# Optimization experiments

Hardware: AMD Instinct MI355X
Metric: run time of the kernel (lower is better)

## Reference

```python
import jax, jax.numpy as jnp
import numpy as np

KER = 8  # patch size used by unfold/fold
EPS = 1e-5


def _gelu(x):
    return jax.nn.gelu(x, approximate=False)  # torch nn.GELU default (exact erf)


def _conv(x, w, b):
    # x: [B,C,H,W], w: [O,I,kh,kw]
    y = jax.lax.conv_general_dilated(x, w, (1, 1), 'SAME',
                                     dimension_numbers=('NCHW', 'OIHW', 'NCHW'))
    return y + b[None, :, None, None]


def _unfold_t(x):
    # F.unfold(k=8, s=8).transpose(1,2): [B,C,H,W] -> [B, L, C*k*k]
    B, C, H, W = x.shape
    Hp, Wp = H // KER, W // KER
    x = x.reshape(B, C, Hp, KER, Wp, KER)
    x = x.transpose(0, 2, 4, 1, 3, 5)  # [B,Hp,Wp,C,k,k]
    return x.reshape(B, Hp * Wp, C * KER * KER)


def _fold(y, H, W):
    # inverse of unfold (non-overlapping): [B,L,C*k*k] -> [B,C,H,W]
    B, L, D = y.shape
    Hp, Wp = H // KER, W // KER
    C = D // (KER * KER)
    y = y.reshape(B, Hp, Wp, C, KER, KER).transpose(0, 3, 1, 4, 2, 5)
    return y.reshape(B, C, H, W)


def _bn1d(x, gamma, beta):
    # BatchNorm1d (training-mode batch stats) on [B, C, L]: stats over (B, L)
    m = x.mean(axis=(0, 2), keepdims=True)
    v = x.var(axis=(0, 2), keepdims=True)  # biased variance, matches torch fwd
    return (x - m) * jax.lax.rsqrt(v + EPS) * gamma[None, :, None] + beta[None, :, None]


def setup_inputs() -> dict:
    key = jax.random.key(0)
    ks = jax.random.split(key, 12)
    B, C, H, W = 4, 64, 256, 256
    dq = KER * KER * C  # 4096

    def n(k, shape, scale=0.02):
        return jax.random.normal(k, shape, jnp.float32) * scale

    return {
        'feat': jax.random.normal(ks[0], (B, C, H, W), jnp.float32),
        'w_enc': n(ks[1], (C, C, 3, 3)), 'b_enc': jnp.zeros((C,), jnp.float32),
        'w_kc': n(ks[2], (C, C, 3, 3)), 'b_kc': jnp.zeros((C,), jnp.float32),
        'w_vc': n(ks[3], (C, C, 3, 3)), 'b_vc': jnp.zeros((C,), jnp.float32),
        'wq': n(ks[4], (1024, dq)), 'bq': jnp.zeros((1024,), jnp.float32),
        'wk': n(ks[5], (1024, dq)), 'bk': jnp.zeros((1024,), jnp.float32),
        'gq': jnp.ones((1024,), jnp.float32), 'betaq': jnp.zeros((1024,), jnp.float32),
        'gk': jnp.ones((1024,), jnp.float32), 'betak': jnp.zeros((1024,), jnp.float32),
        'w_f1': n(ks[6], (4 * C, C, 1, 1)), 'b_f1': jnp.zeros((4 * C,), jnp.float32),
        'w_f2': n(ks[7], (C, 4 * C, 1, 1)), 'b_f2': jnp.zeros((C,), jnp.float32),
    }


def reference(feat, w_enc, b_enc, w_kc, b_kc, w_vc, b_vc, wq, bq, wk, bk,
              gq, betaq, gk, betak, w_f1, b_f1, w_f2, b_f2):
    H, W = feat.shape[-2:]
    refer = _gelu(_conv(feat, w_enc, b_enc))
    feat_k = _gelu(_conv(feat, w_kc, b_kc))
    feat_v = _gelu(_conv(feat, w_vc, b_vc))

    q_un = _unfold_t(refer)   # [B,L,4096]
    k_un = _unfold_t(feat_k)
    v_un = _unfold_t(feat_v)

    # Linear -> BN1d over 1024 channels (transpose dance as in the torch code)
    qp = _bn1d((q_un @ wq.T + bq).transpose(0, 2, 1), gq, betaq).transpose(0, 2, 1)  # [B,L,1024]
    kp = _bn1d((k_un @ wk.T + bk).transpose(0, 2, 1), gk, betak).transpose(0, 2, 1)  # [B,L,1024]

    scale = jnp.sqrt(jnp.asarray(qp.shape[2], qp.dtype))
    scores = jnp.einsum('bld,bmd->blm', qp, kp) / scale  # [B,L,L]
    attn = jax.nn.softmax(scores, axis=2)
    out = jnp.einsum('blm,bmd->bld', attn, v_un)  # [B,L,4096]

    out = _fold(out, H, W)  # [B,C,H,W]
    ff = _gelu(_conv(out, w_f1, b_f1))
    ff = _gelu(_conv(ff, w_f2, b_f2))
    return ff + feat
```

## Files before the change

### kernel.cpp

```cpp
#include <hip/hip_runtime.h>
#include <hip/hip_bf16.h>

typedef unsigned short u16;
typedef __attribute__((ext_vector_type(8))) short short8v;
typedef __attribute__((ext_vector_type(8))) unsigned short u16x8;
typedef __attribute__((ext_vector_type(4))) float f32x4;

#define HWPIX 65536
#define AS1(p) ((const __attribute__((address_space(1))) void*)(p))
#define AS3(p) ((__attribute__((address_space(3))) void*)(p))

__device__ __forceinline__ float bfbits2f(u16 u) {
  return __uint_as_float(((unsigned)u) << 16);
}
__device__ __forceinline__ float4 ld4bf(const u16* p) {
  ushort4 u = *(const ushort4*)(const void*)p;
  return make_float4(bfbits2f(u.x), bfbits2f(u.y), bfbits2f(u.z), bfbits2f(u.w));
}
__device__ __forceinline__ u16 f2bf(float f) {
  union { __hip_bfloat16 h; u16 u; } c;
  c.h = __float2bfloat16(f);
  return c.u;
}
__device__ __forceinline__ float gelu_f(float x) {
  float z = 0.79788456f * x * (1.0f + 0.044715f * x * x);
  float e = __expf(2.0f * z);
  float th = 1.0f - 2.0f * __builtin_amdgcn_rcpf(e + 1.0f);
  return 0.5f * x * (1.0f + th);
}
__device__ __forceinline__ u16x8 bn8(u16x8 v, const float* __restrict__ sc,
                                     const float* __restrict__ sh, int kk) {
  float4 s0 = *(const float4*)&sc[kk], s1 = *(const float4*)&sc[kk + 4];
  float4 t0 = *(const float4*)&sh[kk], t1 = *(const float4*)&sh[kk + 4];
  u16x8 r;
  r[0] = f2bf(bfbits2f(v[0]) * s0.x + t0.x); r[1] = f2bf(bfbits2f(v[1]) * s0.y + t0.y);
  r[2] = f2bf(bfbits2f(v[2]) * s0.z + t0.z); r[3] = f2bf(bfbits2f(v[3]) * s0.w + t0.w);
  r[4] = f2bf(bfbits2f(v[4]) * s1.x + t1.x); r[5] = f2bf(bfbits2f(v[5]) * s1.y + t1.y);
  r[6] = f2bf(bfbits2f(v[6]) * s1.z + t1.z); r[7] = f2bf(bfbits2f(v[7]) * s1.w + t1.w);
  return r;
}

__launch_bounds__(256)
__global__ void prep_k(const float* __restrict__ feat, u16* __restrict__ featb,
                       const float* __restrict__ w0, const float* __restrict__ w1,
                       const float* __restrict__ w2, const float* __restrict__ b0,
                       const float* __restrict__ b1, const float* __restrict__ b2,
                       const float* __restrict__ wf1, const float* __restrict__ wf2,
                       u16* __restrict__ wT, float* __restrict__ bias192,
                       u16* __restrict__ wf1b, u16* __restrict__ wf2b) {
  __shared__ float tile[64][65];
  const int t = threadIdx.x;
  const int bxg = blockIdx.x;
  if (bxg < 4096) {
    const int xs = (bxg & 3) << 6, yy = (bxg >> 2) & 255, b = bxg >> 10;
#pragma unroll
    for (int it = 0; it < 4; ++it) {
      const int idx = t + it * 256;
      const int c = idx >> 4, seg = (idx & 15) << 2;
      float4 v = *(const float4*)&feat[(((size_t)(b * 64 + c)) << 16) + yy * 256 + xs + seg];
      tile[c][seg] = v.x; tile[c][seg + 1] = v.y; tile[c][seg + 2] = v.z; tile[c][seg + 3] = v.w;
    }
    __syncthreads();
#pragma unroll
    for (int it = 0; it < 4; ++it) {
      const int idx = t + it * 256;
      const int cs = (idx & 15) << 2, px = idx >> 4;
      ushort4 r;
      r.x = f2bf(tile[cs + 0][px]); r.y = f2bf(tile[cs + 1][px]);
      r.z = f2bf(tile[cs + 2][px]); r.w = f2bf(tile[cs + 3][px]);
      *(ushort4*)&featb[(((size_t)((b * 256 + yy) * 256 + xs + px)) << 6) + cs] = r;
    }
    return;
  }
  const int bx = bxg - 4096;
  if (bx >= 497) {
    const int e = (bx - 497) * 256 + t;
    wf2b[e] = f2bf(wf2[e]);
    return;
  }
  if (bx >= 433) {
    const int e = (bx - 433) * 256 + t;
    wf1b[e] = f2bf(wf1[e]);
    return;
  }
  if (bx == 432) {
    if (t < 192) {
      const float* bp = (t < 64) ? b0 : (t < 128) ? b1 : b2;
      bias192[t] = bp[t & 63];
    }
    return;
  }
  const int e = bx * 256 + t;
  const int pos = e / 12288, rem = e % 12288;
  const int n = rem >> 6, ic = rem & 63;
  const int conv = n >> 6, oc = n & 63;
  const float* wp = (conv == 0) ? w0 : (conv == 1) ? w1 : w2;
  wT[e] = f2bf(wp[(oc * 64 + ic) * 9 + pos]);
}

__launch_bounds__(256)
__global__ void wcvt2_k(const float* __restrict__ s0, u16* __restrict__ d0,
                        const float* __restrict__ s1, u16* __restrict__ d1) {
  const float* src = blockIdx.y ? s1 : s0;
  u16* dst = blockIdx.y ? d1 : d0;
  const int i = (blockIdx.x * 256 + threadIdx.x) << 2;
  float4 v = *(const float4*)&src[i];
  ushort4 r;
  r.x = f2bf(v.x); r.y = f2bf(v.y); r.z = f2bf(v.z); r.w = f2bf(v.w);
  *(ushort4*)&dst[i] = r;
}

__launch_bounds__(256)
__global__ void convmfma_k(const u16* __restrict__ featb, const u16* __restrict__ wT,
                           const float* __restrict__ bias192, u16* __restrict__ qun,
                           u16* __restrict__ kun, u16* __restrict__ vT) {
  __shared__ u16 As[128 * 64];
  __shared__ u16 Bs[192 * 64];
  const int tid = threadIdx.x;
  const int lin = blockIdx.x;
  const int virt = (lin & 7) * 256 + (lin >> 3);
  const int b = virt >> 9, yy = (virt >> 1) & 255, x0 = (virt & 1) << 7;
  const int lane = tid & 63, w = tid >> 6;
  const int wm = w >> 1, wn = w & 1;

  u16x8 rA[4], rB[6];
  auto issue = [&](int pos) {
    const int dy = pos / 3, dx = pos % 3;
    const int yp = yy + dy - 1;
    const bool yok = (unsigned)yp < 256u;
#pragma unroll
    for (int i = 0; i < 4; ++i) {
      const int slot = tid + (i << 8);
      const int row = slot >> 3, cg = slot & 7;
      const int xp = x0 + row + dx - 1;
      u16x8 v{};
      if (yok && (unsigned)xp < 256u)
        v = *(const u16x8*)&featb[(((size_t)((b * 256 + yp) * 256 + xp)) << 6) + (cg << 3)];
      rA[i] = v;
    }
    const u16* wb = wT + (size_t)pos * 12288;
#pragma unroll
    for (int i = 0; i < 6; ++i) {
      const int slot = tid + (i << 8);
      const int row = slot >> 3, cg = slot & 7;
      rB[i] = *(const u16x8*)&wb[(row << 6) + (cg << 3)];
    }
  };
  auto commit = [&]() {
#pragma unroll
    for (int i = 0; i < 4; ++i) {
      const int slot = tid + (i << 8);
      const int row = slot >> 3, cg = slot & 7;
      *(u16x8*)&As[(row << 6) + ((cg ^ (row & 7)) << 3)] = rA[i];
    }
#pragma unroll
    for (int i = 0; i < 6; ++i) {
      const int slot = tid + (i << 8);
      const int row = slot >> 3, cg = slot & 7;
      *(u16x8*)&Bs[(row << 6) + ((cg ^ (row & 7)) << 3)] = rB[i];
    }
  };

  f32x4 acc[4][6] = {};
  const int kc = (lane >> 4) << 3;
  const int afr = wm * 64 + (lane & 15);
  const int bfr0 = wn * 96 + (lane & 15);

  issue(0);
  commit();
  __syncthreads();

  for (int pos = 0; pos < 9; ++pos) {
    if (pos + 1 < 9) issue(pos + 1);
#pragma unroll
    for (int ks = 0; ks < 2; ++ks) {
      const int ce = (ks << 5) + kc;
      short8v a[4], bf[6];
#pragma unroll
      for (int f = 0; f < 4; ++f) {
        const int row = afr + f * 16;
        a[f] = *(const short8v*)&As[(row << 6) + (ce ^ ((row & 7) << 3))];
      }
#pragma unroll
      for (int f = 0; f < 6; ++f) {
        const int row = bfr0 + f * 16;
        bf[f] = *(const short8v*)&Bs[(row << 6) + (ce ^ ((row & 7) << 3))];
      }
#pragma unroll
      for (int i = 0; i < 4; ++i)
#pragma unroll
        for (int j = 0; j < 6; ++j)
          acc[i][j] = __builtin_amdgcn_mfma_f32_16x16x32_bf16(a[i], bf[j], acc[i][j], 0, 0, 0);
    }
    __syncthreads();
    if (pos + 1 < 9) {
      commit();
      __syncthreads();
    }
  }

  const int py = yy >> 3, ky = yy & 7;
  const int rp0 = wm * 64 + ((lane >> 4) << 2);
#pragma unroll
  for (int j = 0; j < 6; ++j) {
    const int colb = wn * 96 + j * 16;
    const int conv = colb >> 6;
    const int oc = (colb & 63) + (lane & 15);
    const float bj = bias192[colb + (lane & 15)];
#pragma unroll
    for (int i = 0; i < 4; ++i) {
      const int rp = rp0 + i * 16;
      const int xg = x0 + rp;
      const int px = xg >> 3, kx0 = xg & 7;
      float v0 = gelu_f(acc[i][j][0] + bj);
      float v1 = gelu_f(acc[i][j][1] + bj);
      float v2 = gelu_f(acc[i][j][2] + bj);
      float v3 = gelu_f(acc[i][j][3] + bj);
      const int d0 = (oc << 6) + (ky << 3) + kx0;
      if (conv < 2) {
        u16* dst = conv ? kun : qun;
        const size_t addr = (((size_t)((b << 10) + py * 32 + px)) << 12) + d0;
        ushort4 r4;
        r4.x = f2bf(v0); r4.y = f2bf(v1); r4.z = f2bf(v2); r4.w = f2bf(v3);
        *(ushort4*)&dst[addr] = r4;
      } else {
        const int m = py * 32 + px;
        const size_t base = (((size_t)(b * 4096 + d0)) << 10) + m;
        vT[base] = f2bf(v0);
        vT[base + 1024] = f2bf(v1);
        vT[base + 2048] = f2bf(v2);
        vT[base + 3072] = f2bf(v3);
      }
    }
  }
}

__launch_bounds__(256)
__global__ void bnpart_k(const u16* __restrict__ q, const u16* __restrict__ k,
                         float2* __restrict__ part) {
  const u16* x = blockIdx.y ? k : q;
  const int b = blockIdx.x, t = threadIdx.x;
  const int c = t << 2;
  float s0 = 0.f, s1 = 0.f, s2 = 0.f, s3 = 0.f;
  float q0 = 0.f, q1 = 0.f, q2 = 0.f, q3 = 0.f;
  const u16* base = x + ((size_t)b << 15) + c;
#pragma unroll 4
  for (int r = 0; r < 32; ++r) {
    float4 v = ld4bf(base + (r << 10));
    s0 += v.x; q0 += v.x * v.x;
    s1 += v.y; q1 += v.y * v.y;
    s2 += v.z; q2 += v.z * v.z;
    s3 += v.w; q3 += v.w * v.w;
  }
  float2* dst = part + (((size_t)(blockIdx.y * 128 + b)) << 10) + c;
  dst[0] = make_float2(s0, q0);
  dst[1] = make_float2(s1, q1);
  dst[2] = make_float2(s2, q2);
  dst[3] = make_float2(s3, q3);
}
__launch_bounds__(256)
__global__ void bnfin_k(const float2* __restrict__ part, const float* __restrict__ gq,
                        const float* __restrict__ betaq, const float* __restrict__ gk,
                        const float* __restrict__ betak, float* __restrict__ scq,
                        float* __restrict__ shq, float* __restrict__ sck,
                        float* __restrict__ shk) {
  const int n = blockIdx.x * 256 + threadIdx.x;
  const int y = blockIdx.y;
  const float2* p = part + (((size_t)(y * 128)) << 10) + n;
  float S = 0.f, S2 = 0.f;
  for (int i = 0; i < 128; ++i) {
    float2 v = p[(size_t)i << 10];
    S += v.x; S2 += v.y;
  }
  const float mean = S * (1.0f / 4096.0f);
  const float var = S2 * (1.0f / 4096.0f) - mean * mean;
  const float rstd = rsqrtf(var + 1e-5f);
  const float g = (y ? gk : gq)[n];
  const float be = (y ? betak : betaq)[n];
  const float sc = g * rstd;
  (y ? sck : scq)[n] = sc;
  (y ? shk : shq)[n] = be - mean * sc;
}

__launch_bounds__(256)
__global__ void softmax_k(u16* __restrict__ s) {
  u16* p = s + (size_t)blockIdx.x * 1024;
  const int tid = threadIdx.x;
  float4 v = ld4bf(p + (tid << 2));
  float mx = fmaxf(fmaxf(v.x, v.y), fmaxf(v.z, v.w));
#pragma unroll
  for (int off = 32; off > 0; off >>= 1) mx = fmaxf(mx, __shfl_xor(mx, off));
  __shared__ float red[8];
  if ((tid & 63) == 0) red[tid >> 6] = mx;
  __syncthreads();
  mx = fmaxf(fmaxf(red[0], red[1]), fmaxf(red[2], red[3]));
  float e0 = __expf(v.x - mx), e1 = __expf(v.y - mx), e2 = __expf(v.z - mx), e3 = __expf(v.w - mx);
  float sm = e0 + e1 + e2 + e3;
#pragma unroll
  for (int off = 32; off > 0; off >>= 1) sm += __shfl_xor(sm, off);
  if ((tid & 63) == 0) red[4 + (tid >> 6)] = sm;
  __syncthreads();
  sm = red[4] + red[5] + red[6] + red[7];
  float inv = 1.0f / sm;
  ushort4 r;
  r.x = f2bf(e0 * inv); r.y = f2bf(e1 * inv); r.z = f2bf(e2 * inv); r.w = f2bf(e3 * inv);
  *(ushort4*)&p[tid << 2] = r;
}

template <int MODE>
__launch_bounds__(512)
__global__ void mgemmL_k(const u16* __restrict__ Ap0, const u16* __restrict__ Bp0,
                         const float* __restrict__ bias0, u16* __restrict__ Cp0, int K,
                         const u16* __restrict__ Ap2, const u16* __restrict__ Bp2,
                         const float* __restrict__ bias2, u16* __restrict__ Cp2) {
  constexpr int SD = (MODE == 0) ? 4096 : 1024;
  __shared__ u16 As[2][128 * 32];
  __shared__ u16 Bs[2][128 * 32];
  const int tid = threadIdx.x;

  int bx, by, z;
  if constexpr (MODE == 2) {
    int lin = blockIdx.x + 32 * blockIdx.y + 256 * blockIdx.z;
    int sw = (lin & 7) * 128 + (lin >> 3);
    bx = sw & 31; by = (sw >> 5) & 7; z = sw >> 8;
  } else {
    bx = blockIdx.x; by = blockIdx.y; z = blockIdx.z;
  }
  const u16* Ap = Ap0;
  const u16* Bp = Bp0;
  const float* bias = bias0;
  u16* Cp = Cp0;
  if constexpr (MODE == 0) {
    if (z) { Ap = Ap2; Bp = Bp2; bias = bias2; Cp = Cp2; }
  }
  const int m0 = by * 128, n0 = bx * 128;
  const int lane = tid & 63, w = tid >> 6;
  const int wm = w >> 2, wn = w & 3;

  const int srow = tid >> 2;
  const int scol = (((tid & 3) ^ ((srow >> 1) & 3)) << 3);
  const size_t zoffA = (MODE == 0) ? 0 : ((size_t)z << 10);
  const size_t zoffB = (MODE == 0) ? 0 : ((size_t)z << 12);
  const u16* gA = Ap + (zoffA + m0 + srow) * (size_t)SD + scol;
  const u16* gB = Bp + (zoffB + n0 + srow) * (size_t)SD + scol;
  const int lwb = w * 512;

  const int NT = K >> 5;
  __builtin_amdgcn_global_load_lds(AS1(gA), AS3(&As[0][lwb]), 16, 0, 0);
  __builtin_amdgcn_global_load_lds(AS1(gB), AS3(&Bs[0][lwb]), 16, 0, 0);

  f32x4 acc[4][2] = {};
  const int fr = lane & 15;
  const int kg = (lane >> 4) << 3;
  const int colsw = kg ^ (((fr >> 1) & 3) << 3);
  int cur = 0;
  for (int t = 0; t < NT; ++t) {
    __syncthreads();
    if (t + 1 < NT) {
      const int kn = (t + 1) << 5;
      __builtin_amdgcn_global_load_lds(AS1(gA + kn), AS3(&As[cur ^ 1][lwb]), 16, 0, 0);
      __builtin_amdgcn_global_load_lds(AS1(gB + kn), AS3(&Bs[cur ^ 1][lwb]), 16, 0, 0);
    }
    const u16* Asb = As[cur];
    const u16* Bsb = Bs[cur];
    short8v a[4], bfr[2];
#pragma unroll
    for (int f = 0; f < 4; ++f)
      a[f] = *(const short8v*)&Asb[(wm * 64 + fr + f * 16) * 32 + colsw];
#pragma unroll
    for (int f = 0; f < 2; ++f)
      bfr[f] = *(const short8v*)&Bsb[(wn * 32 + fr + f * 16) * 32 + colsw];
#pragma unroll
    for (int i = 0; i < 4; ++i)
#pragma unroll
      for (int j = 0; j < 2; ++j)
        acc[i][j] = __builtin_amdgcn_mfma_f32_16x16x32_bf16(a[i], bfr[j], acc[i][j], 0, 0, 0);
    cur ^= 1;
  }

  const int rowbase = m0 + wm * 64 + ((lane >> 4) << 2);
  const int colbase = n0 + wn * 32 + (lane & 15);
  if constexpr (MODE == 2) {
    const size_t coff = (size_t)(8 + 8 * z) * 524288;
    u16* C = Cp + coff;
#pragma unroll
    for (int j = 0; j < 2; ++j) {
      const int d = colbase + j * 16;
      const int c = d >> 6, ky = (d >> 3) & 7, kx = d & 7;
#pragma unroll
      for (int i = 0; i < 4; ++i)
#pragma unroll
        for (int r = 0; r < 4; ++r) {
          const int l = rowbase + i * 16 + r;
          const int p = (((l >> 5) << 3) + ky) * 256 + ((l & 31) << 3) + kx;
          C[((size_t)p << 6) + c] = f2bf(acc[i][j][r]);
        }
    }
  } else {
#pragma unroll
    for (int j = 0; j < 2; ++j) {
      const int col = colbase + j * 16;
      const float bj = bias[col];
#pragma unroll
      for (int i = 0; i < 4; ++i)
#pragma unroll
        for (int r = 0; r < 4; ++r)
          Cp[(size_t)(rowbase + i * 16 + r) * 1024 + col] = f2bf(acc[i][j][r] + bj);
    }
  }
}

__launch_bounds__(512)
__global__ void mgemm1_k(const u16* __restrict__ Ap, const u16* __restrict__ Bp,
                         const float* __restrict__ sA, const float* __restrict__ hA,
                         const float* __restrict__ sB, const float* __restrict__ hB,
                         u16* __restrict__ Cp, int K) {
  constexpr int SD = 1024;
  __shared__ u16 As[2][128 * 72];
  __shared__ u16 Bs[2][128 * 72];
  const int tid = threadIdx.x;
  const int bx = blockIdx.x, by = blockIdx.y, z = blockIdx.z;
  const int m0 = by * 128, n0 = bx * 128;
  const int lane = tid & 63, w = tid >> 6;
  const int wm = w >> 2, wn = w & 3;

  const int srow = tid >> 3;
  const int scol = (tid & 7) << 3;
  const size_t zoff = (size_t)z << 10;
  const u16* A0 = Ap + (zoff + m0 + srow) * (size_t)SD + scol;
  const u16* A1 = A0 + (size_t)64 * SD;
  const u16* B0 = Bp + (zoff + n0 + srow) * (size_t)SD + scol;
  const u16* B1 = B0 + (size_t)64 * SD;
  const int l0 = srow * 72 + scol;
  const int l1 = (srow + 64) * 72 + scol;

  const int NT = K >> 6;
  u16x8 pA0 = bn8(*(const u16x8*)A0, sA, hA, scol);
  u16x8 pA1 = bn8(*(const u16x8*)A1, sA, hA, scol);
  u16x8 pB0 = bn8(*(const u16x8*)B0, sB, hB, scol);
  u16x8 pB1 = bn8(*(const u16x8*)B1, sB, hB, scol);
  *(u16x8*)&As[0][l0] = pA0; *(u16x8*)&As[0][l1] = pA1;
  *(u16x8*)&Bs[0][l0] = pB0; *(u16x8*)&Bs[0][l1] = pB1;
  __syncthreads();

  f32x4 acc[4][2] = {};
  int cur = 0;
  for (int t = 0; t < NT; ++t) {
    const int kn = (t + 1) << 6;
    if (t + 1 < NT) {
      pA0 = *(const u16x8*)(A0 + kn);
      pA1 = *(const u16x8*)(A1 + kn);
      pB0 = *(const u16x8*)(B0 + kn);
      pB1 = *(const u16x8*)(B1 + kn);
    }
    const u16* Asb = As[cur];
    const u16* Bsb = Bs[cur];
#pragma unroll
    for (int ks = 0; ks < 2; ++ks) {
      const int kc = ks * 32 + ((lane >> 4) << 3);
      short8v a[4], bfr[2];
#pragma unroll
      for (int f = 0; f < 4; ++f)
        a[f] = *(const short8v*)&Asb[(wm * 64 + (lane & 15) + f * 16) * 72 + kc];
#pragma unroll
      for (int f = 0; f < 2; ++f)
        bfr[f] = *(const short8v*)&Bsb[(wn * 32 + (lane & 15) + f * 16) * 72 + kc];
#pragma unroll
      for (int i = 0; i < 4; ++i)
#pragma unroll
        for (int j = 0; j < 2; ++j)
          acc[i][j] = __builtin_amdgcn_mfma_f32_16x16x32_bf16(a[i], bfr[j], acc[i][j], 0, 0, 0);
    }
    if (t + 1 < NT) {
      pA0 = bn8(pA0, sA, hA, kn + scol); pA1 = bn8(pA1, sA, hA, kn + scol);
      pB0 = bn8(pB0, sB, hB, kn + scol); pB1 = bn8(pB1, sB, hB, kn + scol);
      *(u16x8*)&As[cur ^ 1][l0] = pA0; *(u16x8*)&As[cur ^ 1][l1] = pA1;
      *(u16x8*)&Bs[cur ^ 1][l0] = pB0; *(u16x8*)&Bs[cur ^ 1][l1] = pB1;
    }
    __syncthreads();
    cur ^= 1;
  }

  const int rowbase = m0 + wm * 64 + ((lane >> 4) << 2);
  const int colbase = n0 + wn * 32 + (lane & 15);
#pragma unroll
  for (int j = 0; j < 2; ++j) {
    const int col = colbase + j * 16;
#pragma unroll
    for (int i = 0; i < 4; ++i)
#pragma unroll
      for (int r = 0; r < 4; ++r) {
        const size_t row = ((size_t)z << 10) + rowbase + i * 16 + r;
        Cp[row * 1024 + col] = f2bf(acc[i][j][r] * 0.03125f);
      }
  }
}

__launch_bounds__(512)
__global__ void ffn_k(const u16* __restrict__ fold, const u16* __restrict__ w1b,
                      const u16* __restrict__ w2b, const float* __restrict__ b1,
                      const float* __restrict__ b2, const float* __restrict__ feat,
                      float* __restrict__ out) {
  extern __shared__ u16 sh[];
  u16* Ash = sh;
  u16* W1s = sh + 9216;
  u16* mids = sh;
  const int t = threadIdx.x;
  const int px0 = blockIdx.x << 7;
  const int z = blockIdx.y;
  const u16* fz = fold + ((size_t)z << 22);

  {
    const int row = t >> 2, cs = (t & 3) << 4;
    const u16* src = fz + (((size_t)(px0 + row)) << 6) + cs;
    *(u16x8*)&Ash[row * 72 + cs] = *(const u16x8*)src;
    *(u16x8*)&Ash[row * 72 + cs + 8] = *(const u16x8*)(src + 8);
  }
  {
    const int row = t >> 1, cs = (t & 1) << 5;
    const u16* src = w1b + (((size_t)row) << 6) + cs;
    *(u16x8*)&W1s[row * 72 + cs] = *(const u16x8*)src;
    *(u16x8*)&W1s[row * 72 + cs + 8] = *(const u16x8*)(src + 8);
    *(u16x8*)&W1s[row * 72 + cs + 16] = *(const u16x8*)(src + 16);
    *(u16x8*)&W1s[row * 72 + cs + 24] = *(const u16x8*)(src + 24);
  }
  __syncthreads();

  const int lane = t & 63, w = t >> 6;
  const int kc = (lane >> 4) << 3;
  const int mrow = w * 16 + (lane & 15);
  f32x4 acc1[16] = {};
  short8v a0 = *(const short8v*)&Ash[mrow * 72 + kc];
  short8v a1 = *(const short8v*)&Ash[mrow * 72 + 32 + kc];
#pragma unroll
  for (int n = 0; n < 16; ++n) {
    const int br = n * 16 + (lane & 15);
    short8v b0 = *(const short8v*)&W1s[br * 72 + kc];
    short8v bv = *(const short8v*)&W1s[br * 72 + 32 + kc];
    acc1[n] = __builtin_amdgcn_mfma_f32_16x16x32_bf16(a0, b0, acc1[n], 0, 0, 0);
    acc1[n] = __builtin_amdgcn_mfma_f32_16x16x32_bf16(a1, bv, acc1[n], 0, 0, 0);
  }
  __syncthreads();

  const int mrow0 = w * 16 + ((lane >> 4) << 2);
#pragma unroll
  for (int n = 0; n < 16; ++n) {
    const int col = n * 16 + (lane & 15);
    const float bj = b1[col];
#pragma unroll
    for (int r = 0; r < 4; ++r)
      mids[(mrow0 + r) * 264 + col] = f2bf(gelu_f(acc1[n][r] + bj));
  }
  __syncthreads();

  f32x4 acc2[4] = {};
#pragma unroll
  for (int ks = 0; ks < 8; ++ks) {
    short8v a2 = *(const short8v*)&mids[(w * 16 + (lane & 15)) * 264 + ks * 32 + kc];
#pragma unroll
    for (int n = 0; n < 4; ++n) {
      short8v bv = *(const short8v*)(const void*)&w2b[(size_t)(n * 16 + (lane & 15)) * 256 + ks * 32 + kc];
      acc2[n] = __builtin_amdgcn_mfma_f32_16x16x32_bf16(a2, bv, acc2[n], 0, 0, 0);
    }
  }
#pragma unroll
  for (int n = 0; n < 4; ++n) {
    const int oc = n * 16 + (lane & 15);
    const float bn = b2[oc];
    const int px = px0 + mrow0;
    const size_t base = (((size_t)(z * 64 + oc)) << 16) + px;
    float4 f = *(const float4*)&feat[base];
    float4 rv;
    rv.x = gelu_f(acc2[n][0] + bn) + f.x;
    rv.y = gelu_f(acc2[n][1] + bn) + f.y;
    rv.z = gelu_f(acc2[n][2] + bn) + f.z;
    rv.w = gelu_f(acc2[n][3] + bn) + f.w;
    *(float4*)&out[base] = rv;
  }
}

extern "C" void kernel_launch(void* const* d_in, const int* in_sizes, int n_in,
                              void* d_out, int out_size, void* d_ws, size_t ws_size,
                              hipStream_t stream) {
  const float* feat  = (const float*)d_in[0];
  const float* w_enc = (const float*)d_in[1];
  const float* b_enc = (const float*)d_in[2];
  const float* w_kc  = (const float*)d_in[3];
  const float* b_kc  = (const float*)d_in[4];
  const float* w_vc  = (const float*)d_in[5];
  const float* b_vc  = (const float*)d_in[6];
  const float* wq    = (const float*)d_in[7];
  const float* bq    = (const float*)d_in[8];
  const float* wk    = (const float*)d_in[9];
  const float* bk    = (const float*)d_in[10];
  const float* gq    = (const float*)d_in[11];
  const float* betaq = (const float*)d_in[12];
  const float* gk    = (const float*)d_in[13];
  const float* betak = (const float*)d_in[14];
  const float* w_f1  = (const float*)d_in[15];
  const float* b_f1  = (const float*)d_in[16];
  const float* w_f2  = (const float*)d_in[17];
  const float* b_f2  = (const float*)d_in[18];

  char* ws = (char*)d_ws;
  const size_t MB = (size_t)1 << 20;
  u16*   qun    = (u16*)(ws);
  u16*   kun    = (u16*)(ws + 32 * MB);
  u16*   qlin   = (u16*)(ws + 64 * MB);
  u16*   wqb    = (u16*)(ws + 72 * MB);
  u16*   wT     = (u16*)(ws + 80 * MB);
  float* bias192= (float*)(ws + 80 * MB + 224 * 1024);
  float* scaleq = (float*)(ws + 80 * MB + 232 * 1024);
  float* shiftq = scaleq + 1024;
  float* scalek = shiftq + 1024;
  float* shiftk = scalek + 1024;
  u16*   wf1b   = (u16*)(ws + 80 * MB + 512 * 1024);
  u16*   wf2b   = (u16*)(ws + 80 * MB + 576 * 1024);
  float2* bnpart = (float2*)(ws + 81 * MB);
  u16*   scores = (u16*)(ws);
  u16*   featb  = (u16*)d_out;
  u16*   vT     = (u16*)((char*)d_out + 32 * MB);
  u16*   wkb    = (u16*)d_out;
  u16*   klin   = (u16*)((char*)d_out + 8 * MB);

  const dim3 blk(256);
  const dim3 blk8(512);
  prep_k<<<4657, blk, 0, stream>>>(feat, featb, w_enc, w_kc, w_vc, b_enc, b_kc, b_vc,
                                   w_f1, w_f2, wT, bias192, wf1b, wf2b);
  convmfma_k<<<2048, blk, 0, stream>>>(featb, wT, bias192, qun, kun, vT);
  wcvt2_k<<<dim3(4096, 2), blk, 0, stream>>>(wq, wqb, wk, wkb);
  mgemmL_k<0><<<dim3(8, 32, 2), blk8, 0, stream>>>(qun, wqb, bq, qlin, 4096,
                                                   kun, wkb, bk, klin);
  bnpart_k<<<dim3(128, 2), blk, 0, stream>>>(qlin, klin, bnpart);
  bnfin_k<<<dim3(4, 2), blk, 0, stream>>>(bnpart, gq, betaq, gk, betak, scaleq, shiftq, scalek, shiftk);
  mgemm1_k<<<dim3(8, 8, 4), blk8, 0, stream>>>(qlin, klin, scaleq, shiftq, scalek, shiftk,
                                               scores, 1024);
  softmax_k<<<4096, blk, 0, stream>>>(scores);
  mgemmL_k<2><<<dim3(32, 8, 4), blk8, 0, stream>>>(scores, vT, nullptr, (u16*)ws, 1024,
                                                   nullptr, nullptr, nullptr, nullptr);
  ffn_k<<<dim3(512, 4), blk8, 67584, stream>>>((u16*)(ws + 8 * MB), wf1b, wf2b, b_f1, b_f2, feat, (float*)d_out);
  (void)in_sizes; (void)n_in; (void)out_size; (void)ws_size;
}
```

Before: 472.8 us.

## Deepen GEMM LDS pipeline to four stages with explicit vmcnt waits, swizzle MODE 0 blocks

```diff
diff --git a/kernel.cpp b/kernel.cpp
--- a/kernel.cpp
+++ b/kernel.cpp
@@ -314,8 +314,8 @@
                          const u16* __restrict__ Ap2, const u16* __restrict__ Bp2,
                          const float* __restrict__ bias2, u16* __restrict__ Cp2) {
   constexpr int SD = (MODE == 0) ? 4096 : 1024;
-  __shared__ u16 As[2][128 * 32];
-  __shared__ u16 Bs[2][128 * 32];
+  __shared__ u16 As[4][128 * 32];
+  __shared__ u16 Bs[4][128 * 32];
   const int tid = threadIdx.x;
 
   int bx, by, z;
@@ -323,6 +323,10 @@
     int lin = blockIdx.x + 32 * blockIdx.y + 256 * blockIdx.z;
     int sw = (lin & 7) * 128 + (lin >> 3);
     bx = sw & 31; by = (sw >> 5) & 7; z = sw >> 8;
+  } else if constexpr (MODE == 0) {
+    int lin = blockIdx.x + 8 * blockIdx.y + 256 * blockIdx.z;
+    int sw = (lin & 7) * 64 + (lin >> 3);
+    bx = sw & 7; by = (sw >> 3) & 31; z = sw >> 8;
   } else {
     bx = blockIdx.x; by = blockIdx.y; z = blockIdx.z;
   }
@@ -346,23 +350,32 @@
   const int lwb = w * 512;
 
   const int NT = K >> 5;
-  __builtin_amdgcn_global_load_lds(AS1(gA), AS3(&As[0][lwb]), 16, 0, 0);
-  __builtin_amdgcn_global_load_lds(AS1(gB), AS3(&Bs[0][lwb]), 16, 0, 0);
+#pragma unroll
+  for (int p = 0; p < 3; ++p) {
+    const int kn = p << 5;
+    __builtin_amdgcn_global_load_lds(AS1(gA + kn), AS3(&As[p][lwb]), 16, 0, 0);
+    __builtin_amdgcn_global_load_lds(AS1(gB + kn), AS3(&Bs[p][lwb]), 16, 0, 0);
+  }
 
   f32x4 acc[4][2] = {};
   const int fr = lane & 15;
   const int kg = (lane >> 4) << 3;
   const int colsw = kg ^ (((fr >> 1) & 3) << 3);
-  int cur = 0;
   for (int t = 0; t < NT; ++t) {
-    __syncthreads();
-    if (t + 1 < NT) {
-      const int kn = (t + 1) << 5;
-      __builtin_amdgcn_global_load_lds(AS1(gA + kn), AS3(&As[cur ^ 1][lwb]), 16, 0, 0);
-      __builtin_amdgcn_global_load_lds(AS1(gB + kn), AS3(&Bs[cur ^ 1][lwb]), 16, 0, 0);
-    }
-    const u16* Asb = As[cur];
-    const u16* Bsb = Bs[cur];
+    if (t < NT - 2)       asm volatile("s_waitcnt vmcnt(4)" ::: "memory");
+    else if (t == NT - 2) asm volatile("s_waitcnt vmcnt(2)" ::: "memory");
+    else                  asm volatile("s_waitcnt vmcnt(0)" ::: "memory");
+    __builtin_amdgcn_sched_barrier(0);
+    __builtin_amdgcn_s_barrier();
+    __builtin_amdgcn_sched_barrier(0);
+    if (t + 3 < NT) {
+      const int kn = (t + 3) << 5;
+      const int nb = (t + 3) & 3;
+      __builtin_amdgcn_global_load_lds(AS1(gA + kn), AS3(&As[nb][lwb]), 16, 0, 0);
+      __builtin_amdgcn_global_load_lds(AS1(gB + kn), AS3(&Bs[nb][lwb]), 16, 0, 0);
+    }
+    const u16* Asb = As[t & 3];
+    const u16* Bsb = Bs[t & 3];
     short8v a[4], bfr[2];
 #pragma unroll
     for (int f = 0; f < 4; ++f)
@@ -375,7 +388,6 @@
 #pragma unroll
       for (int j = 0; j < 2; ++j)
         acc[i][j] = __builtin_amdgcn_mfma_f32_16x16x32_bf16(a[i], bfr[j], acc[i][j], 0, 0, 0);
-    cur ^= 1;
   }
 
   const int rowbase = m0 + wm * 64 + ((lane >> 4) << 2);
```

After: 468.3 us. No clear change (-0.9%).
